# Kernel tuning notes

Measured on AMD Instinct MI355X. Metric: run time of the kernel, lower is better.

## Reference

```python
import jax, jax.numpy as jnp
import numpy as np
from jax import lax

K_STEEP = 10.0      # ssm_K: surrogate spike steepness
V_TH_MIN = 0.1      # ssm_v_th_min
EK_FLOOR = 0.01     # ssm_ek_floor


def setup_inputs() -> dict:
    key = jax.random.key(0)
    ks = jax.random.split(key, 11)
    B, T, D, N = 2, 1024, 1024, 16
    s = lambda fan: 1.0 / np.sqrt(fan)
    return {
        "hidden_states": jax.random.normal(ks[0], (B, T, D), jnp.float32),
        "W_xz": jax.random.normal(ks[1], (D, 2 * D), jnp.float32) * s(D),
        "W_dt": jax.random.normal(ks[2], (D, D), jnp.float32) * s(D),
        "b_dt": jax.random.normal(ks[3], (D,), jnp.float32) * 0.1,
        "A_log": jax.random.uniform(ks[4], (D, N), jnp.float32, 0.0, 1.0),
        "W_B": jax.random.normal(ks[5], (D, N), jnp.float32) * s(D),
        "W_C": jax.random.normal(ks[6], (D, N), jnp.float32) * s(D),
        "D_skip": jax.random.normal(ks[7], (D,), jnp.float32) * 0.1,
        "W_out": jax.random.normal(ks[8], (D, D), jnp.float32) * s(D),
        "v_th": jax.random.uniform(ks[9], (D,), jnp.float32, 0.0, 0.5),
    }


def _bio_ssm(h, W_xz, W_dt, b_dt, A_log, W_B, W_C, D_skip, W_out, v_th):
    # h: (T, B, D) time-major, as in the torch wrapper after permute(1,0,2)
    T, B, D = h.shape
    N = A_log.shape[1]
    xz = jnp.einsum('tbd,de->tbe', h, W_xz)
    x, z = jnp.split(xz, 2, axis=-1)                       # (T,B,D) each
    dt = jax.nn.softplus(jnp.einsum('tbd,de->tbe', x, W_dt) + b_dt)  # (T,B,D)
    A = -jnp.exp(A_log)                                     # (D,N), negative
    Bm = jnp.einsum('tbd,dn->tbn', h, W_B)                  # (T,B,N)
    Cm = jnp.einsum('tbd,dn->tbn', h, W_C)                  # (T,B,N)
    decay = jnp.exp(dt[..., None] * A)                      # (T,B,D,N)
    inp = (dt * x)[..., None] * Bm[:, :, None, :]           # (T,B,D,N)

    def step(s, td):
        dec, ip, c = td
        s = dec * s + ip                                    # (B,D,N)
        y = jnp.einsum('bdn,bn->bd', s, c)
        return s, y

    s0 = jnp.zeros((B, D, N), h.dtype)
    _, y = lax.scan(step, s0, (decay, inp, Cm))             # y: (T,B,D)
    y = y + D_skip * x
    vth = jnp.maximum(v_th, V_TH_MIN)
    spike_p = jax.nn.sigmoid(K_STEEP * (y - vth))           # surrogate spiking gate
    y_sp = y * spike_p
    pc = jnp.mean(spike_p)                                  # ponder cost
    efc = jnp.mean(jax.nn.relu(EK_FLOOR - y * y))           # ek-floor cost
    out = jnp.einsum('tbd,de->tbe', y_sp * jax.nn.silu(z), W_out)
    return out, pc, efc


def reference(hidden_states, W_xz, W_dt, b_dt, A_log, W_B, W_C, D_skip, W_out, v_th):
    h = jnp.transpose(hidden_states, (1, 0, 2))             # (T,B,D)
    h_out, pc, efc = _bio_ssm(h, W_xz, W_dt, b_dt, A_log, W_B, W_C, D_skip, W_out, v_th)
    out = h_out - h                                         # mixer residual delta
    return jnp.transpose(out, (1, 0, 2))                    # (B,T,D)
```

## Files before the change

kernel.cpp:

```cpp
#include <hip/hip_runtime.h>
#include <hip/hip_bf16.h>
#include <stdint.h>

#define TT 1024
#define BB 2
#define DD 1024
#define NN 16
#define NCH 64
#define LCH 16

#define K_STEEP 10.0f
#define V_TH_MIN 0.1f
#define L2E 1.44269504088896f

typedef __bf16 bf16x8 __attribute__((ext_vector_type(8)));
typedef float f32x4 __attribute__((ext_vector_type(4)));

__device__ __forceinline__ short f2bf(float f) {
    union { float f; unsigned u; } c; c.f = f;
    unsigned r = (c.u + 0x7fffu + ((c.u >> 16) & 1u)) >> 16;
    return (short)r;
}
__device__ __forceinline__ float bf2f(short s) {
    union { unsigned u; float f; } c;
    c.u = ((unsigned)(unsigned short)s) << 16;
    return c.f;
}

__device__ __forceinline__ void gload_lds16(const void* g, void* l) {
    __builtin_amdgcn_global_load_lds(
        (const __attribute__((address_space(1))) void*)g,
        (__attribute__((address_space(3))) void*)l, 16, 0, 0);
}

template<int BM, int EPI, bool FUSE_BC>
__global__ __launch_bounds__(256) void gemm_mfma(
    const short* __restrict__ A, int lda,
    const short* __restrict__ BT,
    float* __restrict__ C, int ldc,
    int M, int Ncols, int K,
    const float* __restrict__ bias,
    const float* __restrict__ sub,
    short* __restrict__ bf16out,
    const short* __restrict__ WbcT,
    float* __restrict__ bcout)
{
    constexpr int RI = BM / 32;
    constexpr int AS_SZ = (FUSE_BC && BM * 32 < 2048) ? 2048 : BM * 32;
    __shared__ short As[AS_SZ];
    __shared__ short Bs[128 * 32];

    const int tid = threadIdx.x;
    const int wave = tid >> 6, lane = tid & 63;
    const int kk = (lane >> 4) * 8;
    const int r16 = lane & 15;
    const int wr = wave >> 1, wc = wave & 1;

    if (FUSE_BC && blockIdx.x == gridDim.x - 1) {
        const int bm2 = blockIdx.y * 32;
        f32x4 acc2 = {};
        for (int k0 = 0; k0 < K; k0 += 64) {
            int off = tid * 16;
            int row = off >> 7;
            int ke  = (off & 127) >> 1;
            gload_lds16(A + (size_t)(bm2 + row) * lda + k0 + ke, (char*)As + off);
            gload_lds16(WbcT + (size_t)row * K + k0 + ke, (char*)Bs + off);
            __syncthreads();
            bf16x8 alo = *(const bf16x8*)&As[(wr * 16 + r16) * 64 + kk];
            bf16x8 ahi = *(const bf16x8*)&As[(wr * 16 + r16) * 64 + kk + 32];
            bf16x8 blo = *(const bf16x8*)&Bs[(wc * 16 + r16) * 64 + kk];
            bf16x8 bhi = *(const bf16x8*)&Bs[(wc * 16 + r16) * 64 + kk + 32];
            acc2 = __builtin_amdgcn_mfma_f32_16x16x32_bf16(alo, blo, acc2, 0, 0, 0);
            acc2 = __builtin_amdgcn_mfma_f32_16x16x32_bf16(ahi, bhi, acc2, 0, 0, 0);
            __syncthreads();
        }
        #pragma unroll
        for (int g = 0; g < 4; g++) {
            int row = bm2 + wr * 16 + (lane >> 4) * 4 + g;
            int col = wc * 16 + r16;
            bcout[(size_t)row * 32 + col] = acc2[g];
        }
        return;
    }

    const int bm = blockIdx.y * BM, bn = blockIdx.x * 128;
    f32x4 acc[RI][4] = {};

    for (int k0 = 0; k0 < K; k0 += 32) {
        #pragma unroll
        for (int it = 0; it < 2; it++) {
            int off = it * 4096 + tid * 16;
            int row = off >> 6;
            int ke  = (off & 63) >> 1;
            gload_lds16(BT + (size_t)(bn + row) * K + k0 + ke, (char*)Bs + off);
        }
        if (tid < BM * 4) {
            int off = tid * 16;
            int row = off >> 6;
            int ke  = (off & 63) >> 1;
            gload_lds16(A + (size_t)(bm + row) * lda + k0 + ke, (char*)As + off);
        }
        __syncthreads();

        bf16x8 a[RI], b[4];
        #pragma unroll
        for (int i = 0; i < RI; i++)
            a[i] = *(const bf16x8*)&As[(wr * (BM / 2) + i * 16 + r16) * 32 + kk];
        #pragma unroll
        for (int j = 0; j < 4; j++)
            b[j] = *(const bf16x8*)&Bs[(wc * 64 + j * 16 + r16) * 32 + kk];
        #pragma unroll
        for (int i = 0; i < RI; i++)
            #pragma unroll
            for (int j = 0; j < 4; j++)
                acc[i][j] = __builtin_amdgcn_mfma_f32_16x16x32_bf16(
                    a[i], b[j], acc[i][j], 0, 0, 0);
        __syncthreads();
    }

    #pragma unroll
    for (int i = 0; i < RI; i++) {
        #pragma unroll
        for (int j = 0; j < 4; j++) {
            #pragma unroll
            for (int g = 0; g < 4; g++) {
                int row = bm + wr * (BM / 2) + i * 16 + (lane >> 4) * 4 + g;
                int col = bn + wc * 64 + j * 16 + r16;
                float v = acc[i][j][g];
                if (EPI == 3) {
                    bf16out[(size_t)row * ldc + col] = f2bf(v);
                } else {
                    if (EPI == 1) {
                        v += bias[col];
                        v = fmaxf(v, 0.f) + log1pf(__expf(-fabsf(v)));
                    }
                    if (EPI == 2) {
                        v -= sub[(size_t)row * ldc + col];
                    }
                    C[(size_t)row * ldc + col] = v;
                }
            }
        }
    }
}

__device__ __forceinline__ void tr_tile(
    const float* __restrict__ W, short* __restrict__ WT,
    int K, int N, int k0, int n0, int tid)
{
    __shared__ float t[32][33];
    int r = tid >> 3, q = tid & 7;
    float4 v = *(const float4*)&W[(size_t)(k0 + r) * N + n0 + q * 4];
    t[r][q * 4 + 0] = v.x; t[r][q * 4 + 1] = v.y;
    t[r][q * 4 + 2] = v.z; t[r][q * 4 + 3] = v.w;
    __syncthreads();
    short4 o = { f2bf(t[q * 4 + 0][r]), f2bf(t[q * 4 + 1][r]),
                 f2bf(t[q * 4 + 2][r]), f2bf(t[q * 4 + 3][r]) };
    *(short4*)&WT[(size_t)(n0 + r) * K + k0 + q * 4] = o;
}

__global__ __launch_bounds__(256) void prep_all(
    const float* __restrict__ H,    short* __restrict__ Hb,
    const float* __restrict__ W_xz, short* __restrict__ WxzT,
    const float* __restrict__ W_dt, short* __restrict__ WdtT,
    const float* __restrict__ W_out,short* __restrict__ WoutT,
    const float* __restrict__ W_B,  const float* __restrict__ W_C,
    short* __restrict__ WbcT)
{
    int bid = blockIdx.x, tid = threadIdx.x;
    if (bid < 2048) {
        int i = bid * 1024 + tid * 4;
        float4 v = *(const float4*)&H[i];
        short4 o = { f2bf(v.x), f2bf(v.y), f2bf(v.z), f2bf(v.w) };
        *(short4*)&Hb[i] = o;
    } else if (bid < 4096) {
        int t = bid - 2048;
        tr_tile(W_xz, WxzT, DD, 2 * DD, (t >> 6) * 32, (t & 63) * 32, tid);
    } else if (bid < 5120) {
        int t = bid - 4096;
        tr_tile(W_dt, WdtT, DD, DD, (t >> 5) * 32, (t & 31) * 32, tid);
    } else if (bid < 6144) {
        int t = bid - 5120;
        tr_tile(W_out, WoutT, DD, DD, (t >> 5) * 32, (t & 31) * 32, tid);
    } else {
        int g = (bid - 6144) * 256 + tid;
        int k = g & (DD - 1);
        int n = g >> 10;
        float v = (n < 16) ? W_B[(size_t)k * NN + n]
                           : W_C[(size_t)k * NN + n - 16];
        WbcT[(size_t)n * DD + k] = f2bf(v);
    }
}

__global__ __launch_bounds__(512) void scan_fused(
    const short* __restrict__ xzb,
    const float* __restrict__ dtb,
    const float* __restrict__ bc,
    const float* __restrict__ A_log,
    const float* __restrict__ D_skip,
    const float* __restrict__ v_th,
    short* __restrict__ gout)
{
    __shared__ float Ls[8][NCH][NN];
    __shared__ float Sd[8][NCH];

    const int tid = threadIdx.x;
    const int dl = tid & 7;
    const int c  = tid >> 3;
    const int d  = blockIdx.x * 8 + dl;
    const int b  = blockIdx.y;
    const int r0 = b * TT + c * LCH;

    float a2[NN];
    #pragma unroll
    for (int n = 0; n < NN; n++)
        a2[n] = -__expf(A_log[(size_t)d * NN + n]) * L2E;

    float s[NN];
    #pragma unroll
    for (int n = 0; n < NN; n++) s[n] = 0.f;
    float sum_dt = 0.f;

    for (int j = 0; j < LCH; j++) {
        int r = r0 + j;
        float dt = dtb[(size_t)r * DD + d];
        float x  = bf2f(xzb[(size_t)r * (2 * DD) + d]);
        float dtx = dt * x;
        sum_dt += dt;
        float bB[NN];
        *(float4*)&bB[0]  = *(const float4*)&bc[(size_t)r * 32 + 0];
        *(float4*)&bB[4]  = *(const float4*)&bc[(size_t)r * 32 + 4];
        *(float4*)&bB[8]  = *(const float4*)&bc[(size_t)r * 32 + 8];
        *(float4*)&bB[12] = *(const float4*)&bc[(size_t)r * 32 + 12];
        #pragma unroll
        for (int n = 0; n < NN; n++) {
            float dec = exp2f(a2[n] * dt);
            s[n] = fmaf(dec, s[n], dtx * bB[n]);
        }
    }
    #pragma unroll
    for (int n = 0; n < NN; n++) Ls[dl][c][n] = s[n];
    Sd[dl][c] = sum_dt;
    __syncthreads();

    if (tid < 128) {
        int dl2 = tid >> 4, n2 = tid & 15;
        float a2n = -__expf(A_log[(size_t)(blockIdx.x * 8 + dl2) * NN + n2]) * L2E;
        float ss = 0.f;
        for (int cc = 0; cc < NCH; cc++) {
            float P = exp2f(a2n * Sd[dl2][cc]);
            float L = Ls[dl2][cc][n2];
            Ls[dl2][cc][n2] = ss;
            ss = fmaf(P, ss, L);
        }
    }
    __syncthreads();

    #pragma unroll
    for (int n = 0; n < NN; n++) s[n] = Ls[dl][c][n];

    float dsk = D_skip[d];
    float vth = fmaxf(v_th[d], V_TH_MIN);

    for (int j = 0; j < LCH; j++) {
        int r = r0 + j;
        float dt = dtb[(size_t)r * DD + d];
        float x  = bf2f(xzb[(size_t)r * (2 * DD) + d]);
        float z  = bf2f(xzb[(size_t)r * (2 * DD) + DD + d]);
        float dtx = dt * x;
        float bB[NN], bC[NN];
        *(float4*)&bB[0]  = *(const float4*)&bc[(size_t)r * 32 + 0];
        *(float4*)&bB[4]  = *(const float4*)&bc[(size_t)r * 32 + 4];
        *(float4*)&bB[8]  = *(const float4*)&bc[(size_t)r * 32 + 8];
        *(float4*)&bB[12] = *(const float4*)&bc[(size_t)r * 32 + 12];
        *(float4*)&bC[0]  = *(const float4*)&bc[(size_t)r * 32 + 16];
        *(float4*)&bC[4]  = *(const float4*)&bc[(size_t)r * 32 + 20];
        *(float4*)&bC[8]  = *(const float4*)&bc[(size_t)r * 32 + 24];
        *(float4*)&bC[12] = *(const float4*)&bc[(size_t)r * 32 + 28];
        float y = 0.f;
        #pragma unroll
        for (int n = 0; n < NN; n++) {
            float dec = exp2f(a2[n] * dt);
            s[n] = fmaf(dec, s[n], dtx * bB[n]);
            y = fmaf(s[n], bC[n], y);
        }
        y = fmaf(dsk, x, y);
        float sp = 1.f / (1.f + __expf(-K_STEEP * (y - vth)));
        float sz = z / (1.f + __expf(-z));
        gout[(size_t)r * DD + d] = f2bf(y * sp * sz);
    }
}

extern "C" void kernel_launch(void* const* d_in, const int* in_sizes, int n_in,
                              void* d_out, int out_size, void* d_ws, size_t ws_size,
                              hipStream_t stream) {
    const float* H      = (const float*)d_in[0];
    const float* W_xz   = (const float*)d_in[1];
    const float* W_dt   = (const float*)d_in[2];
    const float* b_dt   = (const float*)d_in[3];
    const float* A_log  = (const float*)d_in[4];
    const float* W_B    = (const float*)d_in[5];
    const float* W_C    = (const float*)d_in[6];
    const float* D_skip = (const float*)d_in[7];
    const float* W_out  = (const float*)d_in[8];
    const float* v_th   = (const float*)d_in[9];
    float* out = (float*)d_out;

    float* ws  = (float*)d_ws;
    float* dtb = ws;
    float* bcb = dtb + 2097152;
    short* p16   = (short*)(bcb + 65536);
    short* xzb   = p16;
    short* Hb    = xzb   + 4194304;
    short* WxzT  = Hb    + 2097152;
    short* WdtT  = WxzT  + 2097152;
    short* WoutT = WdtT  + 1048576;
    short* WbcT  = WoutT + 1048576;
    short* gb    = WbcT  + 32768;

    const int M = BB * TT;

    prep_all<<<6272, 256, 0, stream>>>(
        H, Hb, W_xz, WxzT, W_dt, WdtT, W_out, WoutT, W_B, W_C, WbcT);
    gemm_mfma<32, 3, true><<<dim3(17, M / 32), 256, 0, stream>>>(
        Hb, DD, WxzT, nullptr, 2 * DD, M, 2 * DD, DD,
        nullptr, nullptr, xzb, WbcT, bcb);
    gemm_mfma<32, 1, false><<<dim3(8, M / 32), 256, 0, stream>>>(
        xzb, 2 * DD, WdtT, dtb, DD, M, DD, DD,
        b_dt, nullptr, nullptr, nullptr, nullptr);
    scan_fused<<<dim3(DD / 8, BB), 512, 0, stream>>>(
        xzb, dtb, bcb, A_log, D_skip, v_th, gb);
    gemm_mfma<32, 2, false><<<dim3(8, M / 32), 256, 0, stream>>>(
        gb, DD, WoutT, out, DD, M, DD, DD,
        nullptr, H, nullptr, nullptr, nullptr);
}
```

Before: 118.4 us.

## Transpose xz and dt to channel-major so the scan reads contiguous vectors

The first GEMM now writes x in row-major bf16 for the dt GEMM and also writes a transposed channel-major copy of xz. The dt GEMM is computed transposed (W_dt^T times x^T) so dt comes out channel-major with the bias applied per row. The scan kernel remaps threads and preloads each chunk's dt, x and z as contiguous vector loads instead of strided per-timestep loads. This removes uncoalesced strided accesses in the scan, at the cost of extra scattered short4 transposed stores in the first GEMM epilogue and an extra x buffer.

```diff
diff --git a/kernel.cpp b/kernel.cpp
--- a/kernel.cpp
+++ b/kernel.cpp
@@ -36,12 +36,13 @@
 template<int BM, int EPI, bool FUSE_BC>
 __global__ __launch_bounds__(256) void gemm_mfma(
     const short* __restrict__ A, int lda,
-    const short* __restrict__ BT,
+    const short* __restrict__ BT, int ldb,
     float* __restrict__ C, int ldc,
     int M, int Ncols, int K,
     const float* __restrict__ bias,
     const float* __restrict__ sub,
-    short* __restrict__ bf16out,
+    short* __restrict__ xb_out,
+    short* __restrict__ xzT_out,
     const short* __restrict__ WbcT,
     float* __restrict__ bcout)
 {
@@ -92,7 +93,7 @@
             int off = it * 4096 + tid * 16;
             int row = off >> 6;
             int ke  = (off & 63) >> 1;
-            gload_lds16(BT + (size_t)(bn + row) * K + k0 + ke, (char*)Bs + off);
+            gload_lds16(BT + (size_t)(bn + row) * ldb + k0 + ke, (char*)Bs + off);
         }
         if (tid < BM * 4) {
             int off = tid * 16;
@@ -122,16 +123,24 @@
     for (int i = 0; i < RI; i++) {
         #pragma unroll
         for (int j = 0; j < 4; j++) {
-            #pragma unroll
-            for (int g = 0; g < 4; g++) {
-                int row = bm + wr * (BM / 2) + i * 16 + (lane >> 4) * 4 + g;
-                int col = bn + wc * 64 + j * 16 + r16;
-                float v = acc[i][j][g];
-                if (EPI == 3) {
-                    bf16out[(size_t)row * ldc + col] = f2bf(v);
-                } else {
-                    if (EPI == 1) {
-                        v += bias[col];
+            int row0 = bm + wr * (BM / 2) + i * 16 + (lane >> 4) * 4;
+            int col = bn + wc * 64 + j * 16 + r16;
+            if (EPI == 3) {
+                short4 p;
+                #pragma unroll
+                for (int g = 0; g < 4; g++) {
+                    short h = f2bf(acc[i][j][g]);
+                    ((short*)&p)[g] = h;
+                    if (col < DD) xb_out[(size_t)(row0 + g) * DD + col] = h;
+                }
+                *(short4*)&xzT_out[(size_t)col * 2048 + row0] = p;
+            } else {
+                #pragma unroll
+                for (int g = 0; g < 4; g++) {
+                    int row = row0 + g;
+                    float v = acc[i][j][g];
+                    if (EPI == 4) {
+                        v += bias[row];
                         v = fmaxf(v, 0.f) + log1pf(__expf(-fabsf(v)));
                     }
                     if (EPI == 2) {
@@ -192,9 +201,9 @@
     }
 }
 
-__global__ __launch_bounds__(512) void scan_fused(
-    const short* __restrict__ xzb,
-    const float* __restrict__ dtb,
+__global__ __launch_bounds__(512) void scan_fused2(
+    const float* __restrict__ dtT,
+    const short* __restrict__ xzT,
     const float* __restrict__ bc,
     const float* __restrict__ A_log,
     const float* __restrict__ D_skip,
@@ -205,12 +214,27 @@
     __shared__ float Sd[8][NCH];
 
     const int tid = threadIdx.x;
-    const int dl = tid & 7;
-    const int c  = tid >> 3;
+    const int c  = (tid & 7) | ((tid >> 6) << 3);
+    const int dl = (tid >> 3) & 7;
     const int d  = blockIdx.x * 8 + dl;
     const int b  = blockIdx.y;
     const int r0 = b * TT + c * LCH;
 
+    float dtv[LCH];
+    {
+        const float* p = &dtT[(size_t)d * 2048 + b * TT + c * LCH];
+        *(float4*)&dtv[0]  = *(const float4*)&p[0];
+        *(float4*)&dtv[4]  = *(const float4*)&p[4];
+        *(float4*)&dtv[8]  = *(const float4*)&p[8];
+        *(float4*)&dtv[12] = *(const float4*)&p[12];
+    }
+    short xv[LCH];
+    {
+        const short* p = &xzT[(size_t)d * 2048 + b * TT + c * LCH];
+        *(int4*)&xv[0] = *(const int4*)&p[0];
+        *(int4*)&xv[8] = *(const int4*)&p[8];
+    }
+
     float a2[NN];
     #pragma unroll
     for (int n = 0; n < NN; n++)
@@ -222,16 +246,16 @@
     float sum_dt = 0.f;
 
     for (int j = 0; j < LCH; j++) {
-        int r = r0 + j;
-        float dt = dtb[(size_t)r * DD + d];
-        float x  = bf2f(xzb[(size_t)r * (2 * DD) + d]);
+        float dt = dtv[j];
+        float x  = bf2f(xv[j]);
         float dtx = dt * x;
         sum_dt += dt;
+        const float* bp = &bc[(size_t)(r0 + j) * 32];
         float bB[NN];
-        *(float4*)&bB[0]  = *(const float4*)&bc[(size_t)r * 32 + 0];
-        *(float4*)&bB[4]  = *(const float4*)&bc[(size_t)r * 32 + 4];
-        *(float4*)&bB[8]  = *(const float4*)&bc[(size_t)r * 32 + 8];
-        *(float4*)&bB[12] = *(const float4*)&bc[(size_t)r * 32 + 12];
+        *(float4*)&bB[0]  = *(const float4*)&bp[0];
+        *(float4*)&bB[4]  = *(const float4*)&bp[4];
+        *(float4*)&bB[8]  = *(const float4*)&bp[8];
+        *(float4*)&bB[12] = *(const float4*)&bp[12];
         #pragma unroll
         for (int n = 0; n < NN; n++) {
             float dec = exp2f(a2[n] * dt);
@@ -259,24 +283,31 @@
     #pragma unroll
     for (int n = 0; n < NN; n++) s[n] = Ls[dl][c][n];
 
+    short zv[LCH];
+    {
+        const short* p = &xzT[(size_t)(DD + d) * 2048 + b * TT + c * LCH];
+        *(int4*)&zv[0] = *(const int4*)&p[0];
+        *(int4*)&zv[8] = *(const int4*)&p[8];
+    }
+
     float dsk = D_skip[d];
     float vth = fmaxf(v_th[d], V_TH_MIN);
 
     for (int j = 0; j < LCH; j++) {
-        int r = r0 + j;
-        float dt = dtb[(size_t)r * DD + d];
-        float x  = bf2f(xzb[(size_t)r * (2 * DD) + d]);
-        float z  = bf2f(xzb[(size_t)r * (2 * DD) + DD + d]);
+        float dt = dtv[j];
+        float x  = bf2f(xv[j]);
+        float z  = bf2f(zv[j]);
         float dtx = dt * x;
+        const float* bp = &bc[(size_t)(r0 + j) * 32];
         float bB[NN], bC[NN];
-        *(float4*)&bB[0]  = *(const float4*)&bc[(size_t)r * 32 + 0];
-        *(float4*)&bB[4]  = *(const float4*)&bc[(size_t)r * 32 + 4];
-        *(float4*)&bB[8]  = *(const float4*)&bc[(size_t)r * 32 + 8];
-        *(float4*)&bB[12] = *(const float4*)&bc[(size_t)r * 32 + 12];
-        *(float4*)&bC[0]  = *(const float4*)&bc[(size_t)r * 32 + 16];
-        *(float4*)&bC[4]  = *(const float4*)&bc[(size_t)r * 32 + 20];
-        *(float4*)&bC[8]  = *(const float4*)&bc[(size_t)r * 32 + 24];
-        *(float4*)&bC[12] = *(const float4*)&bc[(size_t)r * 32 + 28];
+        *(float4*)&bB[0]  = *(const float4*)&bp[0];
+        *(float4*)&bB[4]  = *(const float4*)&bp[4];
+        *(float4*)&bB[8]  = *(const float4*)&bp[8];
+        *(float4*)&bB[12] = *(const float4*)&bp[12];
+        *(float4*)&bC[0]  = *(const float4*)&bp[16];
+        *(float4*)&bC[4]  = *(const float4*)&bp[20];
+        *(float4*)&bC[8]  = *(const float4*)&bp[24];
+        *(float4*)&bC[12] = *(const float4*)&bp[28];
         float y = 0.f;
         #pragma unroll
         for (int n = 0; n < NN; n++) {
@@ -287,7 +318,7 @@
         y = fmaf(dsk, x, y);
         float sp = 1.f / (1.f + __expf(-K_STEEP * (y - vth)));
         float sz = z / (1.f + __expf(-z));
-        gout[(size_t)r * DD + d] = f2bf(y * sp * sz);
+        gout[(size_t)(r0 + j) * DD + d] = f2bf(y * sp * sz);
     }
 }
 
@@ -307,11 +338,12 @@
     float* out = (float*)d_out;
 
     float* ws  = (float*)d_ws;
-    float* dtb = ws;
-    float* bcb = dtb + 2097152;
+    float* dtT = ws;
+    float* bcb = dtT + 2097152;
     short* p16   = (short*)(bcb + 65536);
-    short* xzb   = p16;
-    short* Hb    = xzb   + 4194304;
+    short* xzT   = p16;
+    short* xb    = xzT   + 4194304;
+    short* Hb    = xb    + 2097152;
     short* WxzT  = Hb    + 2097152;
     short* WdtT  = WxzT  + 2097152;
     short* WoutT = WdtT  + 1048576;
@@ -323,14 +355,14 @@
     prep_all<<<6272, 256, 0, stream>>>(
         H, Hb, W_xz, WxzT, W_dt, WdtT, W_out, WoutT, W_B, W_C, WbcT);
     gemm_mfma<32, 3, true><<<dim3(17, M / 32), 256, 0, stream>>>(
-        Hb, DD, WxzT, nullptr, 2 * DD, M, 2 * DD, DD,
-        nullptr, nullptr, xzb, WbcT, bcb);
-    gemm_mfma<32, 1, false><<<dim3(8, M / 32), 256, 0, stream>>>(
-        xzb, 2 * DD, WdtT, dtb, DD, M, DD, DD,
-        b_dt, nullptr, nullptr, nullptr, nullptr);
-    scan_fused<<<dim3(DD / 8, BB), 512, 0, stream>>>(
-        xzb, dtb, bcb, A_log, D_skip, v_th, gb);
-    gemm_mfma<32, 2, false><<<dim3(8, M / 32), 256, 0, stream>>>(
-        gb, DD, WoutT, out, DD, M, DD, DD,
-        nullptr, H, nullptr, nullptr, nullptr);
-}
+        Hb, DD, WxzT, DD, nullptr, 0, M, 2 * DD, DD,
+        nullptr, nullptr, xb, xzT, WbcT, bcb);
+    gemm_mfma<32, 4, false><<<dim3(M / 128, DD / 32), 256, 0, stream>>>(
+        WdtT, DD, xb, DD, dtT, M, DD, M, DD,
+        b_dt, nullptr, nullptr, nullptr, nullptr, nullptr);
+    scan_fused2<<<dim3(DD / 8, BB), 512, 0, stream>>>(
+        dtT, xzT, bcb, A_log, D_skip, v_th, gb);
+    gemm_mfma<32, 2, false><<<dim3(DD / 128, M / 32), 256, 0, stream>>>(
+        gb, DD, WoutT, DD, out, DD, M, DD, DD,
+        nullptr, H, nullptr, nullptr, nullptr, nullptr);
+}
```

Result: slower. 167.1 us (+41.1%).
